# Kernel optimization log

Hardware: AMD Instinct MI355X
Metric: run time of the kernel (lower is better)

The kernel has to match this reference:

```python
import jax, jax.numpy as jnp
import numpy as np

N_EMBD = 1024
HIDDEN = 4 * N_EMBD          # 4096
ADAPT = HIDDEN // 16         # 256
NUM_EXPERTS = 8
B, S = 4, 2048
LN_EPS = 1e-5


def setup_inputs() -> dict:
    key = jax.random.key(0)
    ks = jax.random.split(key, 8)
    x = jax.random.normal(ks[0], (B, S, N_EMBD), dtype=jnp.float32)
    # top-1 routing: one-hot expert weights (disjoint masks, standard MoE dispatch)
    route = jax.random.randint(ks[1], (B, S), 0, NUM_EXPERTS)
    expert_weights = jax.nn.one_hot(route, NUM_EXPERTS, dtype=jnp.float32)
    up_scale = 0.1 / N_EMBD ** 0.5
    adapt_scale0 = 0.1 / HIDDEN ** 0.5
    adapt_scale = 0.01 / ADAPT ** 0.5
    W_up = jax.random.normal(ks[2], (HIDDEN, N_EMBD), dtype=jnp.float32) * up_scale
    W_adapt = jax.random.normal(ks[3], (ADAPT, HIDDEN), dtype=jnp.float32) * adapt_scale0
    W_exp_adapters = jax.random.normal(ks[4], (NUM_EXPERTS, ADAPT, ADAPT), dtype=jnp.float32) * adapt_scale
    ln_gamma = jnp.ones((NUM_EXPERTS, ADAPT), dtype=jnp.float32)
    ln_beta = jnp.zeros((NUM_EXPERTS, ADAPT), dtype=jnp.float32)
    W_expert_proj = jax.random.normal(ks[5], (HIDDEN, ADAPT), dtype=jnp.float32) * adapt_scale
    W_out = jax.random.normal(ks[6], (N_EMBD, HIDDEN), dtype=jnp.float32) * adapt_scale
    return {"x": x, "expert_weights": expert_weights, "W_up": W_up,
            "W_adapt": W_adapt, "W_exp_adapters": W_exp_adapters,
            "ln_gamma": ln_gamma, "ln_beta": ln_beta,
            "W_expert_proj": W_expert_proj, "W_out": W_out}


def reference(x, expert_weights, W_up, W_adapt, W_exp_adapters, ln_gamma, ln_beta, W_expert_proj, W_out):
    b, s, d = x.shape
    T = b * s
    E = expert_weights.shape[-1]
    xt = x.reshape(T, d)

    # shared MLP path (silu(up_proj(x))) -> output_proj
    h = jax.nn.silu(xt @ W_up.T)                      # [T, HIDDEN]
    shared_out = (h @ W_out.T).reshape(b, s, d)       # [B, S, D]

    active = expert_weights.reshape(T, E) > 0         # [T, E]
    any_active = jnp.any(active, axis=-1)             # [T]
    last_idx = E - 1 - jnp.argmax(active[:, ::-1], axis=-1)  # [T]

    # pre_adapt (silu(up) recomputed == h) -> adapt_proj
    a = h @ W_adapt.T                                 # [T, ADAPT]
    # per-expert adapter linears, then select the winning expert per token
    a_all = jnp.einsum('td,eod->teo', a, W_exp_adapters)      # [T, E, ADAPT]
    a_sel = jnp.take_along_axis(a_all, last_idx[:, None, None], axis=1)[:, 0]  # [T, ADAPT]

    # per-expert LayerNorm params gathered per token
    g = ln_gamma[last_idx]                            # [T, ADAPT]
    be = ln_beta[last_idx]
    mu = jnp.mean(a_sel, axis=-1, keepdims=True)
    var = jnp.mean(jnp.square(a_sel - mu), axis=-1, keepdims=True)
    a_norm = (a_sel - mu) * jax.lax.rsqrt(var + LN_EPS) * g + be

    h2 = a_norm @ W_expert_proj.T                     # [T, HIDDEN]
    e_out = h2 @ W_out.T                              # [T, D]
    combined = jnp.where(any_active[:, None], e_out, 0.0).reshape(b, s, d)
    return shared_out + 0.1 * combined
```

## Files before the change

kernel.cpp:

```cpp
#include <hip/hip_runtime.h>
#include <cstdint>

#define TOK  8192
#define DEMB 1024
#define HID  4096
#define ADP  256
#define NEXP 8
#define KAUG 4352

typedef __bf16 bf16x8 __attribute__((ext_vector_type(8)));
typedef float  f32x4  __attribute__((ext_vector_type(4)));

__device__ __forceinline__ unsigned short f2bf(float f) {
  unsigned int u = __float_as_uint(f);
  u += 0x7fffu + ((u >> 16) & 1u);
  return (unsigned short)(u >> 16);
}
__device__ __forceinline__ float bf2f(unsigned short b) {
  return __uint_as_float(((unsigned int)b) << 16);
}

__global__ __launch_bounds__(256) void convert_all(
    const float* __restrict__ x, const float* __restrict__ wup,
    const float* __restrict__ wout, const float* __restrict__ wadapt,
    const float* __restrict__ wexp, const float* __restrict__ ew,
    const float* __restrict__ wp,
    unsigned short* __restrict__ xb, unsigned short* __restrict__ wub,
    unsigned short* __restrict__ wob, unsigned short* __restrict__ wab,
    unsigned short* __restrict__ web, int* __restrict__ route,
    unsigned short* __restrict__ wpT) {
  __shared__ float tile[64][65];
  int b = blockIdx.x;
  if (b >= 8992) {
    int wli = b - 8992;
    const int h0 = (wli & 63) * 64;
    const int a0 = (wli >> 6) * 64;
    const int t = threadIdx.x;
    const int r = t >> 4;
    const int c = (t & 15) * 4;
#pragma unroll
    for (int p = 0; p < 4; ++p) {
      int row = p * 16 + r;
      float4 v = *(const float4*)(wp + (size_t)(h0 + row) * ADP + a0 + c);
      tile[c + 0][row] = v.x;
      tile[c + 1][row] = v.y;
      tile[c + 2][row] = v.z;
      tile[c + 3][row] = v.w;
    }
    __syncthreads();
#pragma unroll
    for (int q = 0; q < 2; ++q) {
      int idx = q * 256 + t;
      int al = idx >> 3;
      int hg = (idx & 7) * 8;
      unsigned int w0 = (unsigned int)f2bf(tile[al][hg + 0]) |
                        ((unsigned int)f2bf(tile[al][hg + 1]) << 16);
      unsigned int w1 = (unsigned int)f2bf(tile[al][hg + 2]) |
                        ((unsigned int)f2bf(tile[al][hg + 3]) << 16);
      unsigned int w2 = (unsigned int)f2bf(tile[al][hg + 4]) |
                        ((unsigned int)f2bf(tile[al][hg + 5]) << 16);
      unsigned int w3 = (unsigned int)f2bf(tile[al][hg + 6]) |
                        ((unsigned int)f2bf(tile[al][hg + 7]) << 16);
      *(uint4*)(wpT + (size_t)(a0 + al) * HID + h0 + hg) =
          make_uint4(w0, w1, w2, w3);
    }
    return;
  }
  if (b >= 8960) {
    int t = (b - 8960) * 256 + threadIdx.x;
    const float* p = ew + (size_t)t * NEXP;
    int r = -1;
#pragma unroll
    for (int e = 0; e < NEXP; ++e)
      if (p[e] > 0.f) r = e;
    route[t] = r;
    return;
  }
  const float* src; unsigned short* dst; int lb; bool strided = false;
  if      (b < 4096) { src = x;      dst = xb;  lb = b; }
  else if (b < 6144) { src = wup;    dst = wub; lb = b - 4096; }
  else if (b < 8192) { src = wout;   dst = wob; lb = b - 6144; strided = true; }
  else if (b < 8704) { src = wadapt; dst = wab; lb = b - 8192; }
  else               { src = wexp;   dst = web; lb = b - 8704; }
  size_t base = (size_t)lb * 2048;
#pragma unroll
  for (int h = 0; h < 2; ++h) {
    size_t off = base + (size_t)h * 1024 + (size_t)threadIdx.x * 4;
    float4 v = *(const float4*)(src + off);
    ushort4 o;
    o.x = f2bf(v.x); o.y = f2bf(v.y); o.z = f2bf(v.z); o.w = f2bf(v.w);
    size_t doff = strided ? (off >> 12) * KAUG + (off & 4095) : off;
    *(ushort4*)(dst + doff) = o;
  }
}

__device__ __forceinline__ void remap_xcd(int li, int gx, int gy,
                                          int& bx, int& by) {
  int xcd = li & 7;
  int slot = li >> 3;
  bx = slot % gx;
  by = xcd * (gy >> 3) + slot / gx;
}

#define PHASE_MID()                                       \
  __builtin_amdgcn_s_barrier();                           \
  asm volatile("s_waitcnt lgkmcnt(0)" ::: "memory");      \
  __builtin_amdgcn_sched_barrier(0);                      \
  __builtin_amdgcn_s_setprio(1)

#define PHASE_END()                                       \
  __builtin_amdgcn_s_setprio(0);                          \
  __builtin_amdgcn_sched_barrier(0);                      \
  __builtin_amdgcn_s_barrier()

#define PHASE_END_VM(N)                                   \
  __builtin_amdgcn_s_setprio(0);                          \
  __builtin_amdgcn_sched_barrier(0);                      \
  asm volatile("s_waitcnt vmcnt(" #N ")" ::: "memory");   \
  __builtin_amdgcn_s_barrier()

template <int MB, int NB>
__device__ __forceinline__ void mfmaQ(const bf16x8 af[4][2], const bf16x8 bf[2][2],
                                      f32x4 acc[8][4]) {
#pragma unroll
  for (int mt = 0; mt < 4; ++mt)
#pragma unroll
    for (int nt = 0; nt < 2; ++nt)
#pragma unroll
      for (int kk = 0; kk < 2; ++kk)
        acc[MB + mt][NB + nt] = __builtin_amdgcn_mfma_f32_16x16x32_bf16(
            af[mt][kk], bf[nt][kk], acc[MB + mt][NB + nt], 0, 0, 0);
}

template <int EPI>
__global__ __launch_bounds__(512, 2) void gemm256(
    const unsigned short* __restrict__ A, int lda,
    const unsigned short* __restrict__ B, int ldb,
    void* __restrict__ C, int ldc, const int* __restrict__ route, int kLen) {
  __shared__ unsigned short As[2][256 * 64];
  __shared__ unsigned short Bs[2][256 * 64];
  const int lane = threadIdx.x & 63;
  const int wave = threadIdx.x >> 6;
  const int wm = wave >> 2, wn = wave & 3;
  int li = blockIdx.x + gridDim.x * blockIdx.y;
  int bx, by;
  remap_xcd(li, gridDim.x, gridDim.y, bx, by);
  const long rowBase = (long)by * 256;
  const long colBase = (long)bx * 256;
  const int srow = lane >> 3;
  const int scol = ((lane & 7) ^ (srow & 7)) * 8;
  const unsigned short* Ag = A + (rowBase + srow) * (long)lda + scol;
  const unsigned short* Bg = B + (colBase + srow) * (long)ldb + scol;
  const int NT = kLen >> 6;

  auto st2 = [&](unsigned short* lds, const unsigned short* g, long ld, int t,
                 int half) {
#pragma unroll
    for (int c = 0; c < 2; ++c) {
      int chunk = half * 16 + wave * 2 + c;
      __builtin_amdgcn_global_load_lds(
          (const __attribute__((address_space(1))) unsigned int*)(uintptr_t)(
              g + (size_t)chunk * 8 * ld + (size_t)t * 64),
          (__attribute__((address_space(3))) unsigned int*)(uintptr_t)(
              lds + chunk * 512),
          16, 0, 0);
    }
  };
  auto rdA = [&](const unsigned short* base, int mhalf, bf16x8 dst[4][2]) {
#pragma unroll
    for (int mt = 0; mt < 4; ++mt)
#pragma unroll
      for (int kk = 0; kk < 2; ++kk) {
        int rr = mhalf * 128 + wm * 64 + mt * 16 + (lane & 15);
        int sw = (kk * 4 + (lane >> 4)) ^ (lane & 7);
        dst[mt][kk] = *(const bf16x8*)&base[rr * 64 + sw * 8];
      }
  };
  auto rdB = [&](const unsigned short* base, int nhalf, bf16x8 dst[2][2]) {
#pragma unroll
    for (int nt = 0; nt < 2; ++nt)
#pragma unroll
      for (int kk = 0; kk < 2; ++kk) {
        int rr = nhalf * 128 + wn * 32 + nt * 16 + (lane & 15);
        int sw = (kk * 4 + (lane >> 4)) ^ (lane & 7);
        dst[nt][kk] = *(const bf16x8*)&base[rr * 64 + sw * 8];
      }
  };

  f32x4 acc[8][4] = {};
  bf16x8 afA[4][2], afB[4][2], bfA[2][2], bfB[2][2];

  st2(As[0], Ag, lda, 0, 0);
  st2(Bs[0], Bg, ldb, 0, 0);
  st2(Bs[0], Bg, ldb, 0, 1);
  st2(As[0], Ag, lda, 0, 1);
  if (NT > 1) {
    st2(As[1], Ag, lda, 1, 0);
    st2(Bs[1], Bg, ldb, 1, 0);
    st2(Bs[1], Bg, ldb, 1, 1);
    st2(As[1], Ag, lda, 1, 1);
  }
  asm volatile("s_waitcnt vmcnt(0)" ::: "memory");
  __builtin_amdgcn_s_barrier();
  rdA(As[0], 0, afA);
  rdB(Bs[0], 0, bfA);
  if (NT > 2) {
    asm volatile("s_waitcnt lgkmcnt(0)" ::: "memory");
    __builtin_amdgcn_s_barrier();
    st2(As[0], Ag, lda, 2, 0);
  }

  for (int t = 0; t < NT; ++t) {
    const int b = t & 1;
    unsigned short* Asn = As[b ^ 1];
    unsigned short* Bsn = Bs[b ^ 1];
    const int s2 = (t + 2 < NT) ? t + 2 : t;
    const int s3 = (t + 3 < NT) ? t + 3 : ((t + 1 < NT) ? t + 1 : t - 1);
    rdB(Bs[b], 1, bfB);
    if (NT > 1) st2(Bs[b], Bg, ldb, s2, 0);
    PHASE_MID();
    mfmaQ<0, 0>(afA, bfA, acc);
    PHASE_END_VM(12);
    rdA(As[b], 1, afB);
    if (NT > 1) st2(Bs[b], Bg, ldb, s2, 1);
    PHASE_MID();
    mfmaQ<0, 2>(afA, bfB, acc);
    PHASE_END_VM(12);
    if (t + 1 < NT) rdA(Asn, 0, afA);
    if (NT > 1) st2(As[b], Ag, lda, s2, 1);
    PHASE_MID();
    mfmaQ<4, 0>(afB, bfA, acc);
    PHASE_END_VM(12);
    if (t + 1 < NT) rdB(Bsn, 0, bfA);
    if (NT > 2) st2(Asn, Ag, lda, s3, 0);
    PHASE_MID();
    mfmaQ<4, 2>(afB, bfB, acc);
    if (t + 1 < NT) { PHASE_END_VM(12); } else { PHASE_END_VM(0); }
  }

  const int rsub = (lane >> 4) * 4;
  const int csub = lane & 15;
#pragma unroll
  for (int mt = 0; mt < 8; ++mt) {
#pragma unroll
    for (int nt = 0; nt < 4; ++nt) {
      long col = colBase + (nt >> 1) * 128 + wn * 32 + (nt & 1) * 16 + csub;
#pragma unroll
      for (int r = 0; r < 4; ++r) {
        long row = rowBase + (mt >> 2) * 128 + wm * 64 + (mt & 3) * 16 + rsub + r;
        float v = acc[mt][nt][r];
        if (EPI == 0) {
          float s = __fdividef(v, 1.0f + __expf(-v));
          ((unsigned short*)C)[row * ldc + col] = f2bf(s);
        } else if (EPI == 1) {
          ((float*)C)[row * ldc + col] = v;
        } else {
          if (route[row] == (int)(col >> 8))
            ((float*)C)[row * ADP + (col & 255)] = v;
        }
      }
    }
  }
}

__device__ __forceinline__ void read_frag4(const unsigned short* base, int lane,
                                           int rowoff, int kk, bf16x8* dst) {
#pragma unroll
  for (int i = 0; i < 4; ++i) {
    int rr = rowoff + i * 16 + (lane & 15);
    int sw = ((kk >> 3) + (lane >> 4)) ^ (lane & 7);
    dst[i] = *(const bf16x8*)&base[rr * 64 + sw * 8];
  }
}

template <int NH>
__device__ __forceinline__ void mfma8(const bf16x8* af, const bf16x8* bf,
                                      f32x4 acc[4][4]) {
#pragma unroll
  for (int mt = 0; mt < 4; ++mt)
#pragma unroll
    for (int q = 0; q < 2; ++q)
      acc[mt][NH * 2 + q] = __builtin_amdgcn_mfma_f32_16x16x32_bf16(
          af[mt], bf[NH * 2 + q], acc[mt][NH * 2 + q], 0, 0, 0);
}

template <int EPI>
__global__ __launch_bounds__(512, 2) void gemm8p(
    const unsigned short* __restrict__ A, int lda,
    const unsigned short* __restrict__ B, int ldb,
    void* __restrict__ C, int ldc, const int* __restrict__ route, int kLen) {
  __shared__ unsigned short As[2][128 * 64];
  __shared__ unsigned short Bs[2][256 * 64];
  const int lane = threadIdx.x & 63;
  const int wave = threadIdx.x >> 6;
  const int wm = wave >> 2, wn = wave & 3;
  int li = blockIdx.x + gridDim.x * blockIdx.y;
  int bx, by;
  remap_xcd(li, gridDim.x, gridDim.y, bx, by);
  const long rowBase = (long)by * 128;
  const long colBase = (long)bx * 256;
  const int srow = lane >> 3;
  const int scol = ((lane & 7) ^ (srow & 7)) * 8;
  const unsigned short* Ag = A + (rowBase + srow) * (long)lda + scol;
  const unsigned short* Bg = B + (colBase + srow) * (long)ldb + scol;
  const int NT = kLen >> 6;

  auto stA = [&](int buf, int t) {
#pragma unroll
    for (int c = 0; c < 2; ++c) {
      int chunk = wave * 2 + c;
      __builtin_amdgcn_global_load_lds(
          (const __attribute__((address_space(1))) unsigned int*)(uintptr_t)(
              Ag + (size_t)chunk * 8 * lda + (size_t)t * 64),
          (__attribute__((address_space(3))) unsigned int*)(uintptr_t)(
              &As[buf][chunk * 512]),
          16, 0, 0);
    }
  };
  auto stB = [&](int buf, int t, int h) {
#pragma unroll
    for (int c = 0; c < 2; ++c) {
      int chunk = h * 16 + wave * 2 + c;
      __builtin_amdgcn_global_load_lds(
          (const __attribute__((address_space(1))) unsigned int*)(uintptr_t)(
              Bg + (size_t)chunk * 8 * ldb + (size_t)t * 64),
          (__attribute__((address_space(3))) unsigned int*)(uintptr_t)(
              &Bs[buf][chunk * 512]),
          16, 0, 0);
    }
  };

  f32x4 acc[4][4] = {};
  bf16x8 af0[4], af1[4], bf0[4], bf1[4];

  stB(0, 0, 0);
  stB(0, 0, 1);
  stA(0, 0);
  if (NT > 1) {
    stA(1, 1);
    stB(1, 1, 0);
    asm volatile("s_waitcnt vmcnt(4)" ::: "memory");
  } else {
    asm volatile("s_waitcnt vmcnt(0)" ::: "memory");
  }
  __builtin_amdgcn_s_barrier();
  read_frag4(&As[0][0], lane, wm * 64, 0, af0);

  for (int t = 0; t < NT; ++t) {
    const int b = t & 1;
    read_frag4(&Bs[b][0], lane, wn * 64, 0, bf0);
    if (t + 1 < NT) stB(b ^ 1, t + 1, 1);
    PHASE_MID();
    mfma8<0>(af0, bf0, acc);
    PHASE_END();
    read_frag4(&As[b][0], lane, wm * 64, 32, af1);
    PHASE_MID();
    mfma8<1>(af0, bf0, acc);
    PHASE_END();
    read_frag4(&Bs[b][0], lane, wn * 64, 32, bf1);
    PHASE_MID();
    mfma8<0>(af1, bf1, acc);
    PHASE_END_VM(4);
    if (t + 1 < NT) read_frag4(&As[b ^ 1][0], lane, wm * 64, 0, af0);
    if (t + 2 < NT) { stA(b, t + 2); stB(b, t + 2, 0); }
    PHASE_MID();
    mfma8<1>(af1, bf1, acc);
    PHASE_END_VM(4);
  }

  const int rsub = (lane >> 4) * 4;
  const int csub = lane & 15;
#pragma unroll
  for (int mt = 0; mt < 4; ++mt) {
#pragma unroll
    for (int nt = 0; nt < 4; ++nt) {
      long col = colBase + wn * 64 + nt * 16 + csub;
#pragma unroll
      for (int r = 0; r < 4; ++r) {
        long row = rowBase + wm * 64 + mt * 16 + rsub + r;
        float v = acc[mt][nt][r];
        if (EPI == 0) {
          float s = __fdividef(v, 1.0f + __expf(-v));
          ((unsigned short*)C)[row * ldc + col] = f2bf(s);
        } else if (EPI == 1) {
          ((float*)C)[row * ldc + col] = v;
        } else {
          if (route[row] == (int)(col >> 8))
            ((float*)C)[row * ADP + (col & 255)] = v;
        }
      }
    }
  }
}

__device__ __forceinline__ void stage_tile(const unsigned short* __restrict__ g,
                                           int ldg, unsigned short* lds,
                                           int wave, int lane) {
  int srow = lane >> 3;
  int scol = ((lane & 7) ^ (srow & 7)) * 8;
#pragma unroll
  for (int c = 0; c < 4; ++c) {
    int chunk = wave * 4 + c;
    const unsigned short* gp = g + (size_t)(chunk * 8 + srow) * ldg + scol;
    unsigned short* lp = lds + chunk * 512;
    __builtin_amdgcn_global_load_lds(
        (const __attribute__((address_space(1))) unsigned int*)(uintptr_t)gp,
        (__attribute__((address_space(3))) unsigned int*)(uintptr_t)lp,
        16, 0, 0);
  }
}

__device__ __forceinline__ void gemm_body1(
    int bxr, int byr, int bz,
    const unsigned short* __restrict__ A, int lda,
    const unsigned short* __restrict__ B, int ldb,
    float* __restrict__ C, int ldc, int kLen, long splitStride,
    unsigned short* As, unsigned short* Bs) {
  const int lane = threadIdx.x & 63;
  const int wave = threadIdx.x >> 6;
  const int wm = wave >> 1, wn = wave & 1;
  const long rowBase = (long)byr * 128;
  const long colBase = (long)bxr * 128;
  const int ks = bz * kLen;
  const unsigned short* Ap = A + rowBase * lda + ks;
  const unsigned short* Bp = B + colBase * ldb + ks;
  f32x4 acc[4][4] = {};

  for (int kt = 0; kt < kLen; kt += 64) {
    stage_tile(Ap + kt, lda, As, wave, lane);
    stage_tile(Bp + kt, ldb, Bs, wave, lane);
    __syncthreads();
#pragma unroll
    for (int kk = 0; kk < 64; kk += 32) {
      const int kb = (kk >> 3) + (lane >> 4);
      const int sw = kb ^ (lane & 7);
      bf16x8 af[4], bfr[4];
#pragma unroll
      for (int mt = 0; mt < 4; ++mt) {
        int m = wm * 64 + mt * 16 + (lane & 15);
        af[mt] = *(const bf16x8*)&As[m * 64 + sw * 8];
      }
#pragma unroll
      for (int nt = 0; nt < 4; ++nt) {
        int n = wn * 64 + nt * 16 + (lane & 15);
        bfr[nt] = *(const bf16x8*)&Bs[n * 64 + sw * 8];
      }
#pragma unroll
      for (int mt = 0; mt < 4; ++mt)
#pragma unroll
        for (int nt = 0; nt < 4; ++nt)
          acc[mt][nt] = __builtin_amdgcn_mfma_f32_16x16x32_bf16(
              af[mt], bfr[nt], acc[mt][nt], 0, 0, 0);
    }
    __syncthreads();
  }

  const int rsub = (lane >> 4) * 4;
  const int csub = lane & 15;
#pragma unroll
  for (int mt = 0; mt < 4; ++mt) {
#pragma unroll
    for (int nt = 0; nt < 4; ++nt) {
      long col = colBase + wn * 64 + nt * 16 + csub;
#pragma unroll
      for (int r = 0; r < 4; ++r) {
        long row = rowBase + wm * 64 + mt * 16 + rsub + r;
        (C + splitStride * bz)[row * ldc + col] = acc[mt][nt][r];
      }
    }
  }
}

__global__ __launch_bounds__(256, 3) void gemm_dual(
    const unsigned short* __restrict__ A0, int lda0,
    const unsigned short* __restrict__ B0, int ldb0,
    float* __restrict__ C0, int ldc0, int kLen0, long ss0, int gx0, int gy0,
    int nb0,
    const unsigned short* __restrict__ A1, int lda1,
    const unsigned short* __restrict__ B1, int ldb1,
    float* __restrict__ C1, int ldc1, int kLen1, long ss1, int gx1, int gy1) {
  __shared__ unsigned short As[128 * 64];
  __shared__ unsigned short Bs[128 * 64];
  int li = blockIdx.x;
  if (li < nb0) {
    int per = gx0 * gy0;
    int z = li / per, rem = li % per;
    int bx, by;
    remap_xcd(rem, gx0, gy0, bx, by);
    gemm_body1(bx, by, z, A0, lda0, B0, ldb0, C0, ldc0, kLen0, ss0, As, Bs);
  } else {
    int wli = li - nb0;
    int per = gx1 * gy1;
    int z = wli / per, rem = wli % per;
    int bx, by;
    remap_xcd(rem, gx1, gy1, bx, by);
    gemm_body1(bx, by, z, A1, lda1, B1, ldb1, C1, ldc1, kLen1, ss1, As, Bs);
  }
}

__global__ __launch_bounds__(256) void reduce_both(
    const float* __restrict__ P, unsigned short* __restrict__ ab,
    const float* __restrict__ Pw, unsigned short* __restrict__ wob) {
  int b = blockIdx.x;
  if (b < 2048) {
    size_t i = ((size_t)b * 256 + threadIdx.x) * 4;
    const size_t stride = (size_t)TOK * ADP;
    float4 p0 = *(const float4*)(P + i);
    float4 p1 = *(const float4*)(P + stride + i);
    float4 p2 = *(const float4*)(P + 2 * stride + i);
    float4 p3 = *(const float4*)(P + 3 * stride + i);
    ushort4 o;
    o.x = f2bf(p0.x + p1.x + p2.x + p3.x);
    o.y = f2bf(p0.y + p1.y + p2.y + p3.y);
    o.z = f2bf(p0.z + p1.z + p2.z + p3.z);
    o.w = f2bf(p0.w + p1.w + p2.w + p3.w);
    *(ushort4*)(ab + i) = o;
  } else {
    size_t i = ((size_t)(b - 2048) * 256 + threadIdx.x) * 4;
    const size_t stride = (size_t)DEMB * ADP;
    float4 s = *(const float4*)(Pw + i);
#pragma unroll
    for (int k = 1; k < 8; ++k) {
      float4 p = *(const float4*)(Pw + k * stride + i);
      s.x += p.x; s.y += p.y; s.z += p.z; s.w += p.w;
    }
    size_t d = i >> 8, a = i & 255;
    ushort4 o;
    o.x = f2bf(0.1f * s.x); o.y = f2bf(0.1f * s.y);
    o.z = f2bf(0.1f * s.z); o.w = f2bf(0.1f * s.w);
    *(ushort4*)(wob + d * KAUG + HID + a) = o;
  }
}

__global__ __launch_bounds__(256) void ln_kernel(
    const float* __restrict__ asel, const int* __restrict__ route,
    const float* __restrict__ gamma, const float* __restrict__ beta,
    unsigned short* __restrict__ haug) {
  const int lane = threadIdx.x & 63;
  const int t = blockIdx.x * 4 + (threadIdx.x >> 6);
  const int e = route[t];
  float4 v = *(const float4*)(asel + (size_t)t * ADP + lane * 4);
  float s1 = v.x + v.y + v.z + v.w;
  float s2 = v.x * v.x + v.y * v.y + v.z * v.z + v.w * v.w;
#pragma unroll
  for (int off = 32; off > 0; off >>= 1) {
    s1 += __shfl_down(s1, off);
    s2 += __shfl_down(s2, off);
  }
  s1 = __shfl(s1, 0);
  s2 = __shfl(s2, 0);
  float mu = s1 * (1.0f / ADP);
  float var = s2 * (1.0f / ADP) - mu * mu;
  float rstd = rsqrtf(var + 1e-5f);
  ushort4 o;
  if (e >= 0) {
    float4 g = *(const float4*)(gamma + (size_t)e * ADP + lane * 4);
    float4 b = *(const float4*)(beta + (size_t)e * ADP + lane * 4);
    o.x = f2bf((v.x - mu) * rstd * g.x + b.x);
    o.y = f2bf((v.y - mu) * rstd * g.y + b.y);
    o.z = f2bf((v.z - mu) * rstd * g.z + b.z);
    o.w = f2bf((v.w - mu) * rstd * g.w + b.w);
  } else {
    o.x = o.y = o.z = o.w = 0;
  }
  *(ushort4*)(haug + (size_t)t * KAUG + HID + lane * 4) = o;
}

extern "C" void kernel_launch(void* const* d_in, const int* in_sizes, int n_in,
                              void* d_out, int out_size, void* d_ws, size_t ws_size,
                              hipStream_t stream) {
  const float* x     = (const float*)d_in[0];
  const float* ew    = (const float*)d_in[1];
  const float* W_up  = (const float*)d_in[2];
  const float* W_ad  = (const float*)d_in[3];
  const float* W_ex  = (const float*)d_in[4];
  const float* gam   = (const float*)d_in[5];
  const float* bet   = (const float*)d_in[6];
  const float* W_pr  = (const float*)d_in[7];
  const float* W_out = (const float*)d_in[8];
  float* out = (float*)d_out;

  char* ws = (char*)d_ws;
  size_t off = 0;
  auto alloc = [&](size_t n) {
    char* p = ws + off;
    off += (n + 255) & ~(size_t)255;
    return p;
  };
  unsigned short* xb   = (unsigned short*)alloc((size_t)TOK * DEMB * 2);
  unsigned short* wub  = (unsigned short*)alloc((size_t)HID * DEMB * 2);
  unsigned short* wob  = (unsigned short*)alloc((size_t)DEMB * KAUG * 2);
  unsigned short* wab  = (unsigned short*)alloc((size_t)ADP * HID * 2);
  unsigned short* web  = (unsigned short*)alloc((size_t)NEXP * ADP * ADP * 2);
  unsigned short* wpT  = (unsigned short*)alloc((size_t)ADP * HID * 2);
  unsigned short* Haug = (unsigned short*)alloc((size_t)TOK * KAUG * 2);
  float*          P    = (float*)alloc((size_t)4 * TOK * ADP * 4);
  float*          Pw   = (float*)alloc((size_t)8 * DEMB * ADP * 4);
  unsigned short* ab   = (unsigned short*)alloc((size_t)TOK * ADP * 2);
  int*          route  = (int*)alloc((size_t)TOK * 4);
  float* asel = P;

  convert_all<<<9248, 256, 0, stream>>>(x, W_up, W_out, W_ad, W_ex, ew, W_pr,
                                        xb, wub, wob, wab, web, route, wpT);
  gemm256<0><<<dim3(HID / 256, TOK / 256, 1), 512, 0, stream>>>(
      xb, DEMB, wub, DEMB, Haug, KAUG, nullptr, DEMB);
  gemm_dual<<<640, 256, 0, stream>>>(
      Haug, KAUG, wab, HID, P, ADP, HID / 4, (long)TOK * ADP, 2, 64, 512,
      wob, KAUG, wpT, HID, Pw, ADP, HID / 8, (long)DEMB * ADP, 2, 8);
  reduce_both<<<2304, 256, 0, stream>>>(P, ab, Pw, wob);
  gemm256<3><<<dim3(NEXP * ADP / 256, TOK / 256, 1), 512, 0, stream>>>(
      ab, ADP, web, ADP, asel, ADP, route, ADP);
  ln_kernel<<<TOK / 4, 256, 0, stream>>>(asel, route, gam, bet, Haug);
  gemm8p<1><<<dim3(DEMB / 256, TOK / 128, 1), 512, 0, stream>>>(
      Haug, KAUG, wob, KAUG, out, DEMB, nullptr, KAUG);
}
```

Baseline: 388.4 us.

## Rework gemm256 pipeline prologue/loop and use 128-tile kernel for expert adapter GEMM

The main 256-tile GEMM's software pipeline is restructured. The prologue now waits only partially on outstanding loads, the loop is unrolled by two with a macro body using fixed double-buffer pointers, and the staging order and vmcnt thresholds are changed. This aims to hide global-to-LDS latency better and drop per-iteration buffer indexing. Separately, the small expert-adapter GEMM (K=256) is moved from the 256-tile kernel to a templated 128-tile kernel with a route-masked epilogue, giving more blocks for better occupancy on a short-K problem.

```diff
diff --git a/kernel.cpp b/kernel.cpp
--- a/kernel.cpp
+++ b/kernel.cpp
@@ -199,44 +199,52 @@
     st2(Bs[1], Bg, ldb, 1, 0);
     st2(Bs[1], Bg, ldb, 1, 1);
     st2(As[1], Ag, lda, 1, 1);
-  }
-  asm volatile("s_waitcnt vmcnt(0)" ::: "memory");
+    asm volatile("s_waitcnt vmcnt(8)" ::: "memory");
+  } else {
+    asm volatile("s_waitcnt vmcnt(0)" ::: "memory");
+  }
   __builtin_amdgcn_s_barrier();
   rdA(As[0], 0, afA);
   rdB(Bs[0], 0, bfA);
-  if (NT > 2) {
-    asm volatile("s_waitcnt lgkmcnt(0)" ::: "memory");
-    __builtin_amdgcn_s_barrier();
-    st2(As[0], Ag, lda, 2, 0);
-  }
-
-  for (int t = 0; t < NT; ++t) {
-    const int b = t & 1;
-    unsigned short* Asn = As[b ^ 1];
-    unsigned short* Bsn = Bs[b ^ 1];
-    const int s2 = (t + 2 < NT) ? t + 2 : t;
-    const int s3 = (t + 3 < NT) ? t + 3 : ((t + 1 < NT) ? t + 1 : t - 1);
-    rdB(Bs[b], 1, bfB);
-    if (NT > 1) st2(Bs[b], Bg, ldb, s2, 0);
-    PHASE_MID();
-    mfmaQ<0, 0>(afA, bfA, acc);
-    PHASE_END_VM(12);
-    rdA(As[b], 1, afB);
-    if (NT > 1) st2(Bs[b], Bg, ldb, s2, 1);
-    PHASE_MID();
-    mfmaQ<0, 2>(afA, bfB, acc);
-    PHASE_END_VM(12);
-    if (t + 1 < NT) rdA(Asn, 0, afA);
-    if (NT > 1) st2(As[b], Ag, lda, s2, 1);
-    PHASE_MID();
-    mfmaQ<4, 0>(afB, bfA, acc);
-    PHASE_END_VM(12);
-    if (t + 1 < NT) rdB(Bsn, 0, bfA);
-    if (NT > 2) st2(Asn, Ag, lda, s3, 0);
-    PHASE_MID();
-    mfmaQ<4, 2>(afB, bfB, acc);
-    if (t + 1 < NT) { PHASE_END_VM(12); } else { PHASE_END_VM(0); }
-  }
+  asm volatile("s_waitcnt lgkmcnt(0)" ::: "memory");
+  __builtin_amdgcn_s_barrier();
+
+#define TBODY(T, AsC, BsC, AsN, BsN)                                         \
+  {                                                                          \
+    const int t_ = (T);                                                      \
+    const int s_ = (t_ + 2 < NT) ? t_ + 2 : t_;                              \
+                                \
+    PHASE_MID();                                                             \
+    rdB(BsC, 1, bfB);                                                        \
+    st2(AsC, Ag, lda, s_, 0);                                                \
+    mfmaQ<0, 0>(afA, bfA, acc);                                              \
+    PHASE_END_VM(10);                                                        \
+                                \
+    PHASE_MID();                                                             \
+    rdA(AsC, 1, afB);                                                        \
+    st2(BsC, Bg, ldb, s_, 0);                                                \
+    mfmaQ<0, 2>(afA, bfB, acc);                                              \
+    PHASE_END_VM(10);                                                        \
+                              \
+    PHASE_MID();                                                             \
+    if (t_ + 1 < NT) rdA(AsN, 0, afA);                                       \
+    st2(BsC, Bg, ldb, s_, 1);                                                \
+    mfmaQ<4, 0>(afB, bfA, acc);                                              \
+    PHASE_END_VM(10);                                                        \
+                              \
+    PHASE_MID();                                                             \
+    if (t_ + 1 < NT) rdB(BsN, 0, bfA);                                       \
+    st2(AsC, Ag, lda, s_, 1);                                                \
+    mfmaQ<4, 2>(afB, bfB, acc);                                              \
+    PHASE_END_VM(10);                                                        \
+  }
+
+  for (int t = 0; t < NT; t += 2) {
+    TBODY(t, As[0], Bs[0], As[1], Bs[1]);
+    TBODY(t + 1, As[1], Bs[1], As[0], Bs[0]);
+  }
+#undef TBODY
+  asm volatile("s_waitcnt vmcnt(0)" ::: "memory");
 
   const int rsub = (lane >> 4) * 4;
   const int csub = lane & 15;
@@ -410,11 +418,13 @@
   }
 }
 
-__device__ __forceinline__ void gemm_body1(
+template <int EPI>
+__device__ __forceinline__ void gemm_body(
     int bxr, int byr, int bz,
     const unsigned short* __restrict__ A, int lda,
     const unsigned short* __restrict__ B, int ldb,
-    float* __restrict__ C, int ldc, int kLen, long splitStride,
+    void* __restrict__ C, int ldc,
+    const int* __restrict__ route, int kLen, long splitStride,
     unsigned short* As, unsigned short* Bs) {
   const int lane = threadIdx.x & 63;
   const int wave = threadIdx.x >> 6;
@@ -465,10 +475,31 @@
 #pragma unroll
       for (int r = 0; r < 4; ++r) {
         long row = rowBase + wm * 64 + mt * 16 + rsub + r;
-        (C + splitStride * bz)[row * ldc + col] = acc[mt][nt][r];
+        float v = acc[mt][nt][r];
+        if (EPI == 1) {
+          ((float*)C + splitStride * bz)[row * ldc + col] = v;
+        } else {
+          if (route[row] == (int)(col >> 8))
+            ((float*)C)[row * ADP + (col & 255)] = v;
+        }
       }
     }
   }
+}
+
+template <int EPI>
+__global__ __launch_bounds__(256, 3) void gemm128(
+    const unsigned short* __restrict__ A, int lda,
+    const unsigned short* __restrict__ B, int ldb,
+    void* __restrict__ C, int ldc,
+    const int* __restrict__ route, int kLen, long splitStride) {
+  __shared__ unsigned short As[128 * 64];
+  __shared__ unsigned short Bs[128 * 64];
+  int li = blockIdx.x + gridDim.x * blockIdx.y;
+  int bx, by;
+  remap_xcd(li, gridDim.x, gridDim.y, bx, by);
+  gemm_body<EPI>(bx, by, blockIdx.z, A, lda, B, ldb, C, ldc, route, kLen,
+                 splitStride, As, Bs);
 }
 
 __global__ __launch_bounds__(256, 3) void gemm_dual(
@@ -487,14 +518,16 @@
     int z = li / per, rem = li % per;
     int bx, by;
     remap_xcd(rem, gx0, gy0, bx, by);
-    gemm_body1(bx, by, z, A0, lda0, B0, ldb0, C0, ldc0, kLen0, ss0, As, Bs);
+    gemm_body<1>(bx, by, z, A0, lda0, B0, ldb0, C0, ldc0, nullptr, kLen0, ss0,
+                 As, Bs);
   } else {
     int wli = li - nb0;
     int per = gx1 * gy1;
     int z = wli / per, rem = wli % per;
     int bx, by;
     remap_xcd(rem, gx1, gy1, bx, by);
-    gemm_body1(bx, by, z, A1, lda1, B1, ldb1, C1, ldc1, kLen1, ss1, As, Bs);
+    gemm_body<1>(bx, by, z, A1, lda1, B1, ldb1, C1, ldc1, nullptr, kLen1, ss1,
+                 As, Bs);
   }
 }
 
@@ -608,8 +641,8 @@
       Haug, KAUG, wab, HID, P, ADP, HID / 4, (long)TOK * ADP, 2, 64, 512,
       wob, KAUG, wpT, HID, Pw, ADP, HID / 8, (long)DEMB * ADP, 2, 8);
   reduce_both<<<2304, 256, 0, stream>>>(P, ab, Pw, wob);
-  gemm256<3><<<dim3(NEXP * ADP / 256, TOK / 256, 1), 512, 0, stream>>>(
-      ab, ADP, web, ADP, asel, ADP, route, ADP);
+  gemm128<3><<<dim3(NEXP * ADP / 128, TOK / 128, 1), 256, 0, stream>>>(
+      ab, ADP, web, ADP, asel, ADP, route, ADP, 0);
   ln_kernel<<<TOK / 4, 256, 0, stream>>>(asel, route, gam, bet, Haug);
   gemm8p<1><<<dim3(DEMB / 256, TOK / 128, 1), 512, 0, stream>>>(
       Haug, KAUG, wob, KAUG, out, DEMB, nullptr, KAUG);
```

Result: no change. 387.3 us (-0.3%).
